# Performance work log

Measured on AMD Instinct MI355X. Metric: run time of the kernel, lower is better.

## Reference

```python
import jax, jax.numpy as jnp
import numpy as np

DIM = 256
NUM_HEADS = 4
HEAD_DIM = DIM // NUM_HEADS


def setup_inputs() -> dict:
    key = jax.random.key(0)
    ks = jax.random.split(key, 8)
    B, N, C = 4, 2048, DIM
    x = jax.random.normal(ks[0], (B, N, C), dtype=jnp.float32)
    R = jax.random.normal(ks[1], (B, 3, 3), dtype=jnp.float32)
    P = jax.random.normal(ks[2], (N, 3), dtype=jnp.float32)
    s = 1.0 / np.sqrt(C)
    qkv_w = jax.random.normal(ks[3], (3 * C, C), dtype=jnp.float32) * s
    qkv_b = jax.random.normal(ks[4], (3 * C,), dtype=jnp.float32) * 0.02
    proj_w = jax.random.normal(ks[5], (C, C), dtype=jnp.float32) * s
    proj_b = jax.random.normal(ks[6], (C,), dtype=jnp.float32) * 0.02
    pos_scale = jnp.asarray(1.0, dtype=jnp.float32)
    return {"x": x, "R": R, "P": P, "qkv_w": qkv_w, "qkv_b": qkv_b,
            "proj_w": proj_w, "proj_b": proj_b, "pos_scale": pos_scale}


def reference(x, R, P, qkv_w, qkv_b, proj_w, proj_b, pos_scale):
    B, N, C = x.shape
    H, D = NUM_HEADS, HEAD_DIM
    scale = D ** -0.5
    # qkv: (B,N,3C) -> (3,B,H,N,D)
    qkv = (x @ qkv_w.T + qkv_b).reshape(B, N, 3, H, D).transpose(2, 0, 3, 1, 4)
    q, k, v = qkv[0], qkv[1], qkv[2]
    # attention logits (B,H,N,N)
    attn = jnp.einsum('bhid,bhjd->bhij', q, k) * scale
    # positional bias: RP = (R @ P^T)^T -> (B,N,3); bias_ij = dot(RP_i, P_j)
    RP = jnp.einsum('bab,jb->bja', R, P) if False else jnp.einsum('bca,ja->bjc', jnp.swapaxes(R, 1, 2), P)
    RP = jnp.einsum('bcd,jd->bjc', R, P)  # (B,N,3): (R @ P.T).T
    bias = jnp.einsum('bik,jk->bij', RP, P)[:, None, :, :] * pos_scale  # (B,1,N,N) broadcast over heads
    attn = jax.nn.softmax(attn + bias, axis=-1)
    out = jnp.einsum('bhij,bhjd->bhid', attn, v)  # (B,H,N,D)
    out = out.transpose(0, 2, 1, 3).reshape(B, N, C)
    out = out @ proj_w.T + proj_b
    return out
```

## Files before the change

### kernel.cpp

```cpp
#include <hip/hip_runtime.h>
#include <hip/hip_bf16.h>

#define B_ 4
#define N_ 2048
#define C_ 256
#define H_ 4
#define D_ 64

typedef __attribute__((ext_vector_type(8))) short bf16x8;
typedef __attribute__((ext_vector_type(4))) float f32x4;

#define LOG2E 1.4426950408889634f

static __device__ inline unsigned short f2bf(float f) {
    unsigned u = __builtin_bit_cast(unsigned, f);
    unsigned r = (u + 0x7fffu + ((u >> 16) & 1u)) >> 16;
    return (unsigned short)r;
}
static __device__ inline float bf2f(unsigned short h) {
    unsigned u = ((unsigned)h) << 16;
    return __builtin_bit_cast(float, u);
}
static __device__ inline unsigned pack2(float a, float b) {
    __hip_bfloat162 h = __float22bfloat162_rn(make_float2(a, b));
    unsigned u;
    __builtin_memcpy(&u, &h, 4);
    return u;
}
static __device__ inline bf16x8 ld_frag(const unsigned short* p) {
    return __builtin_bit_cast(bf16x8, *(const uint4*)p);
}
static __device__ inline void gload_lds16(const unsigned short* g, unsigned short* l) {
    __builtin_amdgcn_global_load_lds(
        (const __attribute__((address_space(1))) unsigned int*)(g),
        (__attribute__((address_space(3))) unsigned int*)(l),
        16, 0, 0);
}
template<int CTRL>
static __device__ inline float fmax_dpp(float x) {
    int yi = __builtin_amdgcn_update_dpp(0, __builtin_bit_cast(int, x),
                                         CTRL, 0xf, 0xf, true);
    return fmaxf(x, __builtin_bit_cast(float, yi));
}

__global__ __launch_bounds__(256) void cvt_kernel(
    const float* __restrict__ x, const float* __restrict__ qkv_w,
    const float* __restrict__ proj_w, const float* __restrict__ Pm,
    unsigned short* __restrict__ xb, unsigned short* __restrict__ wqb,
    unsigned short* __restrict__ wpb, unsigned short* __restrict__ eb)
{
    const int bid = blockIdx.x, tid = threadIdx.x;
    if (bid >= 1152) {
        const int n = (bid - 1152) * 256 + tid;
        const float* pp = Pm + n * 3;
        float p0 = pp[0], p1 = pp[1], p2 = pp[2];
        unsigned u0 = f2bf(p0), u1 = f2bf(p1), u2 = f2bf(p2);
        unsigned v0 = f2bf(p0 - bf2f((unsigned short)u0));
        unsigned v1 = f2bf(p1 - bf2f((unsigned short)u1));
        unsigned v2 = f2bf(p2 - bf2f((unsigned short)u2));
        uint4 lo, hi;
        lo.x = u0 | (u1 << 16); lo.y = u2 | (v0 << 16);
        lo.z = v1 | (v2 << 16); lo.w = u0 | (u1 << 16);
        hi.x = u2; hi.y = 0u; hi.z = 0u; hi.w = 0u;
        *(uint4*)&eb[n * 16 + 0] = lo;
        *(uint4*)&eb[n * 16 + 8] = hi;
        return;
    }
    const float* s; unsigned short* d; int i;
    if (bid < 1024)      { s = x;      d = xb;  i = (bid * 256 + tid) * 8; }
    else if (bid < 1120) { s = qkv_w;  d = wqb; i = ((bid - 1024) * 256 + tid) * 8; }
    else                 { s = proj_w; d = wpb; i = ((bid - 1120) * 256 + tid) * 8; }
    float4 a = *(const float4*)(s + i);
    float4 b = *(const float4*)(s + i + 4);
    uint4 u;
    u.x = pack2(a.x, a.y); u.y = pack2(a.z, a.w);
    u.z = pack2(b.x, b.y); u.w = pack2(b.z, b.w);
    *(uint4*)(d + i) = u;
}

__global__ __launch_bounds__(256) void qkv_gemm(
    const unsigned short* __restrict__ xb, const unsigned short* __restrict__ wb,
    const float* __restrict__ bias, unsigned short* __restrict__ qb,
    unsigned short* __restrict__ kb, unsigned short* __restrict__ vt)
{
    __shared__ __align__(16) unsigned short As[2][128 * 64];
    __shared__ __align__(16) unsigned short Bs[2][128 * 64];
    const int m0 = blockIdx.x * 128, o0 = blockIdx.y * 128;
    const int tid = threadIdx.x;
    const int wave = tid >> 6, lane = tid & 63, quad = lane >> 4, l16 = lane & 15;
    const int wy = wave >> 1, wx = wave & 1;
    const int x7 = l16 & 7;
    const int rl = lane >> 3, sl = lane & 7;
    const int swz = (sl ^ rl) * 8;

    const unsigned short* aq0 = &xb[(size_t)(m0 + 32 * wave + rl) * 256 + swz];
    const unsigned short* bq0 = &wb[(size_t)(o0 + 32 * wave + rl) * 256 + swz];

    auto ISSUE = [&](int buf, int k0) {
        unsigned short* ad = &As[buf][(32 * wave) * 64];
        unsigned short* bd = &Bs[buf][(32 * wave) * 64];
        #pragma unroll
        for (int i = 0; i < 4; ++i) {
            gload_lds16(aq0 + (size_t)(8 * i) * 256 + k0, ad + (8 * i) * 64);
            gload_lds16(bq0 + (size_t)(8 * i) * 256 + k0, bd + (8 * i) * 64);
        }
    };

    f32x4 acc[4][4];
    #pragma unroll
    for (int i = 0; i < 4; ++i)
        #pragma unroll
        for (int j = 0; j < 4; ++j) acc[i][j] = (f32x4){0.f, 0.f, 0.f, 0.f};

    ISSUE(0, 0);

    #pragma unroll
    for (int t = 0; t < 4; ++t) {
        const int cur = t & 1;
        asm volatile("s_waitcnt vmcnt(0)" ::: "memory");
        __builtin_amdgcn_s_barrier();
        __builtin_amdgcn_sched_barrier(0);
        if (t < 3) ISSUE(cur ^ 1, (t + 1) * 64);
        __builtin_amdgcn_s_setprio(1);
        #pragma unroll
        for (int ks = 0; ks < 2; ++ks) {
            bf16x8 a[4], b[4];
            #pragma unroll
            for (int mt = 0; mt < 4; ++mt)
                a[mt] = ld_frag(&As[cur][(wy * 64 + mt * 16 + l16) * 64
                                         + (((ks * 4 + quad) ^ x7) * 8)]);
            #pragma unroll
            for (int nt = 0; nt < 4; ++nt)
                b[nt] = ld_frag(&Bs[cur][(wx * 64 + nt * 16 + l16) * 64
                                         + (((ks * 4 + quad) ^ x7) * 8)]);
            #pragma unroll
            for (int mt = 0; mt < 4; ++mt)
                #pragma unroll
                for (int nt = 0; nt < 4; ++nt)
                    acc[mt][nt] = __builtin_amdgcn_mfma_f32_16x16x32_bf16(a[mt], b[nt], acc[mt][nt], 0, 0, 0);
        }
        __builtin_amdgcn_s_setprio(0);
    }

    const int sec = o0 + wx * 64;
    const int three = sec >> 8;
    const int h = (sec >> 6) & 3;
    const int b = m0 >> 11;
    float bv[4];
    #pragma unroll
    for (int nt = 0; nt < 4; ++nt) bv[nt] = bias[sec + nt * 16 + l16];

    if (three == 2) {
        const int n64 = (m0 + wy * 64) & 2047;
        const size_t bh64 = ((size_t)b * H_ + h) * 64;
        #pragma unroll
        for (int nt = 0; nt < 4; ++nt) {
            int d = nt * 16 + l16;
            #pragma unroll
            for (int r = 0; r < 4; ++r) {
                ushort4 v;
                v.x = f2bf(acc[0][nt][r] + bv[nt]);
                v.y = f2bf(acc[1][nt][r] + bv[nt]);
                v.z = f2bf(acc[2][nt][r] + bv[nt]);
                v.w = f2bf(acc[3][nt][r] + bv[nt]);
                *(ushort4*)&vt[(bh64 + d) * N_ + n64 + 16 * quad + 4 * r] = v;
            }
        }
    } else {
        unsigned short* dst = (three == 0) ? qb : kb;
        float sc = (three == 0) ? (0.125f * LOG2E) : 1.0f;
        #pragma unroll
        for (int mt = 0; mt < 4; ++mt)
            #pragma unroll
            for (int r = 0; r < 4; ++r) {
                int n = (m0 + wy * 64 + mt * 16 + quad * 4 + r) & 2047;
                size_t rowbase = (((size_t)b * H_ + h) * N_ + n) * D_;
                #pragma unroll
                for (int nt = 0; nt < 4; ++nt)
                    dst[rowbase + nt * 16 + l16] = f2bf((acc[mt][nt][r] + bv[nt]) * sc);
            }
    }
}

#define LDK 64

__global__ __launch_bounds__(512) void attn_kernel(
    const unsigned short* __restrict__ qb, const unsigned short* __restrict__ kb,
    const unsigned short* __restrict__ vt, const unsigned short* __restrict__ eb,
    const float* __restrict__ Rm, const float* __restrict__ Pm,
    const float* __restrict__ ps_ptr,
    unsigned short* __restrict__ Opart, float* __restrict__ ml)
{
    __shared__ __align__(16) unsigned short Ks[2][64 * LDK];
    __shared__ __align__(16) unsigned short Vs[64 * LDK];
    __shared__ __align__(16) unsigned short Ps[128 * LDK];

    const int bh = blockIdx.y;
    const int b = bh >> 2;
    const int i0 = blockIdx.x * 128;
    const int split = blockIdx.z;
    const int tid = threadIdx.x;
    const int wave = tid >> 6, lane = tid & 63;
    const int quad = lane >> 4, l16 = lane & 15;
    const int x7 = l16 & 7;
    const float ps = ps_ptr[0];

    const size_t base = (size_t)bh * N_ * D_;
    const unsigned short* qg = qb + base;
    const unsigned short* kg = kb + base;
    const unsigned short* vg = vt + base;

    const int jbeg = split * (N_ / 4);

    const int rl = lane >> 3, sl = lane & 7;
    const int swz = (sl ^ rl) * 8;
    const unsigned short* kq = kg + (size_t)(jbeg + wave * 8 + rl) * D_ + swz;
    const unsigned short* vq = vg + (size_t)(wave * 8 + rl) * N_ + jbeg + swz;
    const unsigned short* ep = eb + (size_t)(jbeg + l16) * 16 + (quad & 1) * 8;

    auto ISSUE_K = [&](int nb) {
        gload_lds16(kq, &Ks[nb][(wave * 8) * LDK]);
        kq += 64 * D_;
    };
    auto ISSUE_V = [&]() {
        gload_lds16(vq, &Vs[(wave * 8) * LDK]);
        vq += 64;
    };
    bf16x8 e[4];
    auto LOAD_E = [&]() {
        #pragma unroll
        for (int t = 0; t < 4; ++t) e[t] = ld_frag(ep + t * 256);
        ep += 64 * 16;
    };

    ISSUE_K(0);
    LOAD_E();

    const int qrow = i0 + wave * 16 + l16;
    bf16x8 aq[3];
    #pragma unroll
    for (int ks = 0; ks < 2; ++ks)
        aq[ks] = ld_frag(&qg[(size_t)qrow * D_ + ks * 32 + quad * 8]);

    {
        float p0 = Pm[qrow * 3 + 0], p1 = Pm[qrow * 3 + 1], p2 = Pm[qrow * 3 + 2];
        float sc = ps * LOG2E;
        unsigned short ah[3], al[3];
        #pragma unroll
        for (int c = 0; c < 3; ++c) {
            float a = (Rm[b * 9 + c * 3 + 0] * p0 + Rm[b * 9 + c * 3 + 1] * p1
                     + Rm[b * 9 + c * 3 + 2] * p2) * sc;
            ah[c] = f2bf(a);
            al[c] = f2bf(a - bf2f(ah[c]));
        }
        bf16x8 ea = (bf16x8){0,0,0,0,0,0,0,0};
        if (quad == 0) {
            ea[0] = (short)ah[0]; ea[1] = (short)ah[1]; ea[2] = (short)ah[2];
            ea[3] = (short)ah[0]; ea[4] = (short)ah[1]; ea[5] = (short)ah[2];
            ea[6] = (short)al[0]; ea[7] = (short)al[1];
        } else if (quad == 1) {
            ea[0] = (short)al[2];
        }
        aq[2] = ea;
    }

    const bf16x8 ones = (bf16x8){0x3F80,0x3F80,0x3F80,0x3F80,0x3F80,0x3F80,0x3F80,0x3F80};

    float m_run = -1e30f;
    f32x4 o_acc[4], lacc;
    #pragma unroll
    for (int t = 0; t < 4; ++t) o_acc[t] = (f32x4){0.f, 0.f, 0.f, 0.f};
    lacc = (f32x4){0.f, 0.f, 0.f, 0.f};

    f32x4 sA[4], sB[4];

    auto S_COMPUTE = [&](f32x4 (&sc)[4], int kb_) {
        __builtin_amdgcn_s_setprio(1);
        #pragma unroll
        for (int t = 0; t < 4; ++t) {
            const int rb = (l16 + 16 * t) * LDK;
            f32x4 c = {0.f, 0.f, 0.f, 0.f};
            #pragma unroll
            for (int ks = 0; ks < 2; ++ks) {
                bf16x8 bk = ld_frag(&Ks[kb_][rb + (((ks * 4 + quad) ^ x7) * 8)]);
                c = __builtin_amdgcn_mfma_f32_16x16x32_bf16(aq[ks], bk, c, 0, 0, 0);
            }
            sc[t] = c;
        }
        #pragma unroll
        for (int t = 0; t < 4; ++t)
            sc[t] = __builtin_amdgcn_mfma_f32_16x16x32_bf16(aq[2], e[t], sc[t], 0, 0, 0);
        __builtin_amdgcn_s_setprio(0);
    };

    auto SOFTMAX = [&](f32x4 (&s)[4]) {
        float mt[4];
        #pragma unroll
        for (int t = 0; t < 4; ++t)
            mt[t] = fmaxf(fmaxf(fmaxf(s[t][0], s[t][1]), s[t][2]), s[t][3]);
        float mx = fmaxf(fmaxf(fmaxf(mt[0], mt[1]), mt[2]), mt[3]);
        mx = fmax_dpp<0xB1>(mx);
        mx = fmax_dpp<0x4E>(mx);
        mx = fmax_dpp<0x124>(mx);
        mx = fmax_dpp<0x128>(mx);
        if (__any(mx > m_run + 8.0f)) {
            float mnew = fmaxf(m_run, mx);
            float alpha = exp2f(m_run - mnew);
            #pragma unroll
            for (int t = 0; t < 4; ++t)
                #pragma unroll
                for (int r = 0; r < 4; ++r)
                    o_acc[t][r] *= alpha;
            #pragma unroll
            for (int r = 0; r < 4; ++r) lacc[r] *= alpha;
            m_run = mnew;
        }
        #pragma unroll
        for (int r = 0; r < 4; ++r) {
            float p0 = exp2f(s[0][r] - m_run), p1 = exp2f(s[1][r] - m_run);
            float p2 = exp2f(s[2][r] - m_run), p3 = exp2f(s[3][r] - m_run);
            uint2 w;
            w.x = pack2(p0, p1);
            w.y = pack2(p2, p3);
            const int prow = quad * 4 + r;
            *(uint2*)&Ps[(wave * 16 + prow) * LDK
                         + (((l16 >> 1) ^ (prow & 7)) * 8) + (l16 & 1) * 4] = w;
        }
    };

    auto PV = [&]() {
        __builtin_amdgcn_s_setprio(1);
        #pragma unroll
        for (int ks = 0; ks < 2; ++ks) {
            bf16x8 ap = ld_frag(&Ps[(wave * 16 + l16) * LDK
                                    + (((ks * 4 + quad) ^ x7) * 8)]);
            #pragma unroll
            for (int t = 0; t < 4; ++t) {
                bf16x8 bv = ld_frag(&Vs[(l16 + 16 * t) * LDK
                                        + (((ks * 4 + quad) ^ x7) * 8)]);
                o_acc[t] = __builtin_amdgcn_mfma_f32_16x16x32_bf16(ap, bv, o_acc[t], 0, 0, 0);
            }
            lacc = __builtin_amdgcn_mfma_f32_16x16x32_bf16(ap, ones, lacc, 0, 0, 0);
        }
        __builtin_amdgcn_s_setprio(0);
    };

    auto STEP = [&](int cur, bool more, f32x4 (&snew)[4], f32x4 (&sold)[4]) {
        asm volatile("s_waitcnt vmcnt(0)" ::: "memory");
        __builtin_amdgcn_s_barrier();
        __builtin_amdgcn_sched_barrier(0);
        LOAD_E();
        ISSUE_V();
        if (more) ISSUE_K(cur ^ 1);
        __builtin_amdgcn_sched_barrier(0);
        SOFTMAX(sold);
        S_COMPUTE(snew, cur);
        __builtin_amdgcn_sched_barrier(0);
        if (more) asm volatile("s_waitcnt vmcnt(1)" ::: "memory");
        else      asm volatile("s_waitcnt vmcnt(0)" ::: "memory");
        __builtin_amdgcn_s_barrier();
        __builtin_amdgcn_sched_barrier(0);
        PV();
    };

    asm volatile("s_waitcnt vmcnt(0)" ::: "memory");
    __builtin_amdgcn_s_barrier();
    __builtin_amdgcn_sched_barrier(0);
    ISSUE_K(1);
    S_COMPUTE(sA, 0);

    #pragma unroll 1
    for (int it = 0; it < 3; ++it) {
        STEP(1, true, sB, sA);
        STEP(0, true, sA, sB);
    }
    STEP(1, false, sB, sA);

    asm volatile("s_waitcnt vmcnt(0)" ::: "memory");
    __builtin_amdgcn_s_barrier();
    __builtin_amdgcn_sched_barrier(0);
    ISSUE_V();
    SOFTMAX(sB);
    asm volatile("s_waitcnt vmcnt(0)" ::: "memory");
    __builtin_amdgcn_s_barrier();
    __builtin_amdgcn_sched_barrier(0);
    PV();

    const size_t pbase = (size_t)(split * 16 + bh) * N_;
    #pragma unroll
    for (int r = 0; r < 4; ++r) {
        int row = i0 + wave * 16 + quad * 4 + r;
        #pragma unroll
        for (int t = 0; t < 4; ++t)
            Opart[(pbase + row) * D_ + l16 + 16 * t] = f2bf(o_acc[t][r]);
        if (l16 == 0) {
            float2* mlp = (float2*)ml;
            mlp[pbase + row] = make_float2(m_run, lacc[r]);
        }
    }
}

__global__ __launch_bounds__(256) void proj_gemm(
    const unsigned short* __restrict__ Opart, const float* __restrict__ ml,
    const unsigned short* __restrict__ wb, const float* __restrict__ bias,
    float* __restrict__ out)
{
    __shared__ __align__(16) unsigned short As[2][64 * 64];
    __shared__ __align__(16) unsigned short Bs[2][64 * 64];
    const int m0 = blockIdx.x * 64, o0 = blockIdx.y * 64;
    const int tid = threadIdx.x;
    const int wave = tid >> 6, lane = tid & 63, quad = lane >> 4, l16 = lane & 15;
    const int x7 = l16 & 7;
    const int rl = lane >> 3, sl = lane & 7;
    const int swz = (sl ^ rl) * 8;
    const float2* mlp = (const float2*)ml;

    const int srow = tid >> 2, sc16 = (tid & 3) * 16;
    const int s0 = (tid & 3) * 2;
    const int sm = m0 + srow, sb = sm >> 11, sn = sm & 2047;

    float wgt[4][4];
    #pragma unroll
    for (int h = 0; h < 4; ++h) {
        size_t r1 = (size_t)(sb * 4 + h) * N_ + sn;
        float2 m0v = mlp[r1], m1v = mlp[r1 + 16 * N_];
        float2 m2v = mlp[r1 + 32 * N_], m3v = mlp[r1 + 48 * N_];
        float mm = fmaxf(fmaxf(m0v.x, m1v.x), fmaxf(m2v.x, m3v.x));
        float w0 = exp2f(m0v.x - mm), w1 = exp2f(m1v.x - mm);
        float w2 = exp2f(m2v.x - mm), w3 = exp2f(m3v.x - mm);
        float inv = 1.f / (m0v.y * w0 + m1v.y * w1 + m2v.y * w2 + m3v.y * w3);
        wgt[h][0] = w0 * inv; wgt[h][1] = w1 * inv;
        wgt[h][2] = w2 * inv; wgt[h][3] = w3 * inv;
    }

    const unsigned short* bq0 = &wb[(size_t)(o0 + 16 * wave + rl) * 256 + swz];
    auto ISSUE_B = [&](int buf, int k0) {
        unsigned short* bd = &Bs[buf][(16 * wave) * 64];
        gload_lds16(bq0 + k0,           bd);
        gload_lds16(bq0 + 8 * 256 + k0, bd + 8 * 64);
    };

    union U16 { uint4 u; unsigned short s[8]; };
    U16 ar[4][2];
    auto LOAD_A = [&](int h) {
        size_t r1 = (size_t)(sb * 4 + h) * N_ + sn;
        #pragma unroll
        for (int s = 0; s < 4; ++s) {
            const unsigned short* p = &Opart[(r1 + (size_t)(16 * s) * N_) * D_ + sc16];
            ar[s][0].u = *(const uint4*)(p);
            ar[s][1].u = *(const uint4*)(p + 8);
        }
    };

    ISSUE_B(0, 0);
    LOAD_A(0);

    f32x4 acc[4];
    #pragma unroll
    for (int j = 0; j < 4; ++j) acc[j] = (f32x4){0.f, 0.f, 0.f, 0.f};

    #pragma unroll
    for (int t = 0; t < 4; ++t) {
        const int cur = t & 1;
        {
            float w0 = wgt[t][0], w1 = wgt[t][1], w2 = wgt[t][2], w3 = wgt[t][3];
            #pragma unroll
            for (int j = 0; j < 2; ++j) {
                uint4 mv;
                unsigned* mp = (unsigned*)&mv;
                #pragma unroll
                for (int q = 0; q < 4; ++q) {
                    float lo = bf2f(ar[0][j].s[2*q])   * w0 + bf2f(ar[1][j].s[2*q])   * w1
                             + bf2f(ar[2][j].s[2*q])   * w2 + bf2f(ar[3][j].s[2*q])   * w3;
                    float hi = bf2f(ar[0][j].s[2*q+1]) * w0 + bf2f(ar[1][j].s[2*q+1]) * w1
                             + bf2f(ar[2][j].s[2*q+1]) * w2 + bf2f(ar[3][j].s[2*q+1]) * w3;
                    mp[q] = pack2(lo, hi);
                }
                *(uint4*)&As[cur][srow * 64 + (((s0 + j) ^ (srow & 7)) * 8)] = mv;
            }
        }
        __syncthreads();
        if (t < 3) {
            ISSUE_B(cur ^ 1, (t + 1) * 64);
            LOAD_A(t + 1);
        }
        __builtin_amdgcn_s_setprio(1);
        #pragma unroll
        for (int ks = 0; ks < 2; ++ks) {
            bf16x8 a = ld_frag(&As[cur][(wave * 16 + l16) * 64
                                        + (((ks * 4 + quad) ^ x7) * 8)]);
            #pragma unroll
            for (int nt = 0; nt < 4; ++nt) {
                bf16x8 b = ld_frag(&Bs[cur][(nt * 16 + l16) * 64
                                            + (((ks * 4 + quad) ^ x7) * 8)]);
                acc[nt] = __builtin_amdgcn_mfma_f32_16x16x32_bf16(a, b, acc[nt], 0, 0, 0);
            }
        }
        __builtin_amdgcn_s_setprio(0);
    }

    float bv[4];
    #pragma unroll
    for (int nt = 0; nt < 4; ++nt) bv[nt] = bias[o0 + nt * 16 + l16];
    #pragma unroll
    for (int r = 0; r < 4; ++r) {
        int m = m0 + wave * 16 + quad * 4 + r;
        #pragma unroll
        for (int nt = 0; nt < 4; ++nt)
            out[(size_t)m * 256 + o0 + nt * 16 + l16] = acc[nt][r] + bv[nt];
    }
}

extern "C" void kernel_launch(void* const* d_in, const int* in_sizes, int n_in,
                              void* d_out, int out_size, void* d_ws, size_t ws_size,
                              hipStream_t stream) {
    const float* x       = (const float*)d_in[0];
    const float* Rm      = (const float*)d_in[1];
    const float* Pm      = (const float*)d_in[2];
    const float* qkv_w   = (const float*)d_in[3];
    const float* qkv_b   = (const float*)d_in[4];
    const float* proj_w  = (const float*)d_in[5];
    const float* proj_b  = (const float*)d_in[6];
    const float* pos_scl = (const float*)d_in[7];
    float* out = (float*)d_out;

    const size_t NE = (size_t)B_ * H_ * N_ * D_;
    unsigned short* opart = (unsigned short*)d_ws;
    unsigned short* qb    = opart + 4 * NE;
    unsigned short* kb    = qb   + NE;
    unsigned short* vtb   = kb   + NE;
    float*          mlb   = (float*)(vtb + NE);
    unsigned short* eb    = (unsigned short*)(mlb + (size_t)4 * 16 * N_ * 2);
    unsigned short* wqb   = eb  + 2048 * 16;
    unsigned short* wpb   = wqb + 768 * 256;
    unsigned short* xb    = opart;

    cvt_kernel<<<1160, 256, 0, stream>>>(x, qkv_w, proj_w, Pm, xb, wqb, wpb, eb);
    qkv_gemm<<<dim3(64, 6), 256, 0, stream>>>(xb, wqb, qkv_b, qb, kb, vtb);
    attn_kernel<<<dim3(16, 16, 4), 512, 0, stream>>>(qb, kb, vtb, eb, Rm, Pm, pos_scl, opart, mlb);
    proj_gemm<<<dim3(128, 4), 256, 0, stream>>>(opart, mlb, wpb, proj_b, out);
}
```

Before: 131.8 us.

## Double KV tile to 128 keys and halve attention split-K count

The attention kernel now processes 128 keys per iteration instead of 64, with larger K/V/P shared buffers and twice the score fragments per wave. The split-K factor drops from 4 to 2, so the grid is half as large and the proj_gemm merge combines only two partial outputs. This cuts loop and barrier overhead and partial-output traffic, but adds register and LDS pressure and leaves fewer blocks to fill the device.

```diff
diff --git a/kernel.cpp b/kernel.cpp
--- a/kernel.cpp
+++ b/kernel.cpp
@@ -183,6 +183,7 @@
 }
 
 #define LDK 64
+#define LDP 128
 
 __global__ __launch_bounds__(512) void attn_kernel(
     const unsigned short* __restrict__ qb, const unsigned short* __restrict__ kb,
@@ -191,9 +192,9 @@
     const float* __restrict__ ps_ptr,
     unsigned short* __restrict__ Opart, float* __restrict__ ml)
 {
-    __shared__ __align__(16) unsigned short Ks[2][64 * LDK];
-    __shared__ __align__(16) unsigned short Vs[64 * LDK];
-    __shared__ __align__(16) unsigned short Ps[128 * LDK];
+    __shared__ __align__(16) unsigned short Ks[2][128 * LDK];
+    __shared__ __align__(16) unsigned short Vs[64 * LDP];
+    __shared__ __align__(16) unsigned short Ps[128 * LDP];
 
     const int bh = blockIdx.y;
     const int b = bh >> 2;
@@ -210,31 +211,33 @@
     const unsigned short* kg = kb + base;
     const unsigned short* vg = vt + base;
 
-    const int jbeg = split * (N_ / 4);
+    const int jbeg = split * (N_ / 2);
 
     const int rl = lane >> 3, sl = lane & 7;
-    const int swz = (sl ^ rl) * 8;
-    const unsigned short* kq = kg + (size_t)(jbeg + wave * 8 + rl) * D_ + swz;
-    const unsigned short* vq = vg + (size_t)(wave * 8 + rl) * N_ + jbeg + swz;
+    const unsigned short* kp = kg + (size_t)(jbeg + wave * 16 + rl) * D_ + (sl ^ rl) * 8;
+    const int rv = lane >> 4, sv = lane & 15;
+    const unsigned short* vp0 = vg + (size_t)(wave * 8 + rv) * N_ + jbeg + (sv ^ rv) * 8;
+    const unsigned short* vp1 = vg + (size_t)(wave * 8 + 4 + rv) * N_ + jbeg + (sv ^ (4 + rv)) * 8;
     const unsigned short* ep = eb + (size_t)(jbeg + l16) * 16 + (quad & 1) * 8;
 
     auto ISSUE_K = [&](int nb) {
-        gload_lds16(kq, &Ks[nb][(wave * 8) * LDK]);
-        kq += 64 * D_;
+        gload_lds16(kp,          &Ks[nb][(wave * 16) * LDK]);
+        gload_lds16(kp + 8 * D_, &Ks[nb][(wave * 16 + 8) * LDK]);
+        kp += 128 * D_;
     };
     auto ISSUE_V = [&]() {
-        gload_lds16(vq, &Vs[(wave * 8) * LDK]);
-        vq += 64;
-    };
-    bf16x8 e[4];
+        gload_lds16(vp0, &Vs[(wave * 8) * LDP]);
+        gload_lds16(vp1, &Vs[(wave * 8 + 4) * LDP]);
+        vp0 += 128; vp1 += 128;
+    };
+    bf16x8 e[8];
     auto LOAD_E = [&]() {
         #pragma unroll
-        for (int t = 0; t < 4; ++t) e[t] = ld_frag(ep + t * 256);
-        ep += 64 * 16;
+        for (int t = 0; t < 8; ++t) e[t] = ld_frag(ep + t * 256);
+        ep += 128 * 16;
     };
 
     ISSUE_K(0);
-    LOAD_E();
 
     const int qrow = i0 + wave * 16 + l16;
     bf16x8 aq[3];
@@ -272,12 +275,12 @@
     for (int t = 0; t < 4; ++t) o_acc[t] = (f32x4){0.f, 0.f, 0.f, 0.f};
     lacc = (f32x4){0.f, 0.f, 0.f, 0.f};
 
-    f32x4 sA[4], sB[4];
-
-    auto S_COMPUTE = [&](f32x4 (&sc)[4], int kb_) {
+    f32x4 sA[8], sB[8];
+
+    auto S_COMPUTE = [&](f32x4 (&sc)[8], int kb_) {
         __builtin_amdgcn_s_setprio(1);
         #pragma unroll
-        for (int t = 0; t < 4; ++t) {
+        for (int t = 0; t < 8; ++t) {
             const int rb = (l16 + 16 * t) * LDK;
             f32x4 c = {0.f, 0.f, 0.f, 0.f};
             #pragma unroll
@@ -288,17 +291,19 @@
             sc[t] = c;
         }
         #pragma unroll
-        for (int t = 0; t < 4; ++t)
+        for (int t = 0; t < 8; ++t)
             sc[t] = __builtin_amdgcn_mfma_f32_16x16x32_bf16(aq[2], e[t], sc[t], 0, 0, 0);
         __builtin_amdgcn_s_setprio(0);
     };
 
-    auto SOFTMAX = [&](f32x4 (&s)[4]) {
-        float mt[4];
-        #pragma unroll
-        for (int t = 0; t < 4; ++t)
+    auto SOFTMAX = [&](f32x4 (&s)[8]) {
+        float mt[8];
+        #pragma unroll
+        for (int t = 0; t < 8; ++t)
             mt[t] = fmaxf(fmaxf(fmaxf(s[t][0], s[t][1]), s[t][2]), s[t][3]);
-        float mx = fmaxf(fmaxf(fmaxf(mt[0], mt[1]), mt[2]), mt[3]);
+        float mx = mt[0];
+        #pragma unroll
+        for (int t = 1; t < 8; ++t) mx = fmaxf(mx, mt[t]);
         mx = fmax_dpp<0xB1>(mx);
         mx = fmax_dpp<0x4E>(mx);
         mx = fmax_dpp<0x124>(mx);
@@ -319,24 +324,28 @@
         for (int r = 0; r < 4; ++r) {
             float p0 = exp2f(s[0][r] - m_run), p1 = exp2f(s[1][r] - m_run);
             float p2 = exp2f(s[2][r] - m_run), p3 = exp2f(s[3][r] - m_run);
-            uint2 w;
-            w.x = pack2(p0, p1);
-            w.y = pack2(p2, p3);
+            float p4 = exp2f(s[4][r] - m_run), p5 = exp2f(s[5][r] - m_run);
+            float p6 = exp2f(s[6][r] - m_run), p7 = exp2f(s[7][r] - m_run);
+            uint2 w0, w1;
+            w0.x = pack2(p0, p1); w0.y = pack2(p2, p3);
+            w1.x = pack2(p4, p5); w1.y = pack2(p6, p7);
             const int prow = quad * 4 + r;
-            *(uint2*)&Ps[(wave * 16 + prow) * LDK
-                         + (((l16 >> 1) ^ (prow & 7)) * 8) + (l16 & 1) * 4] = w;
+            const int a0 = (wave * 16 + prow) * LDP
+                         + (((l16 >> 1) ^ (prow & 7)) * 8) + (l16 & 1) * 4;
+            *(uint2*)&Ps[a0] = w0;
+            *(uint2*)&Ps[a0 + 64] = w1;
         }
     };
 
     auto PV = [&]() {
         __builtin_amdgcn_s_setprio(1);
         #pragma unroll
-        for (int ks = 0; ks < 2; ++ks) {
-            bf16x8 ap = ld_frag(&Ps[(wave * 16 + l16) * LDK
+        for (int ks = 0; ks < 4; ++ks) {
+            bf16x8 ap = ld_frag(&Ps[(wave * 16 + l16) * LDP
                                     + (((ks * 4 + quad) ^ x7) * 8)]);
             #pragma unroll
             for (int t = 0; t < 4; ++t) {
-                bf16x8 bv = ld_frag(&Vs[(l16 + 16 * t) * LDK
+                bf16x8 bv = ld_frag(&Vs[(l16 + 16 * t) * LDP
                                         + (((ks * 4 + quad) ^ x7) * 8)]);
                 o_acc[t] = __builtin_amdgcn_mfma_f32_16x16x32_bf16(ap, bv, o_acc[t], 0, 0, 0);
             }
@@ -345,18 +354,19 @@
         __builtin_amdgcn_s_setprio(0);
     };
 
-    auto STEP = [&](int cur, bool more, f32x4 (&snew)[4], f32x4 (&sold)[4]) {
+    auto STEP = [&](int cur, bool more, f32x4 (&snew)[8], f32x4 (&sold)[8]) {
         asm volatile("s_waitcnt vmcnt(0)" ::: "memory");
         __builtin_amdgcn_s_barrier();
         __builtin_amdgcn_sched_barrier(0);
         LOAD_E();
         ISSUE_V();
+        __builtin_amdgcn_sched_barrier(0);
         if (more) ISSUE_K(cur ^ 1);
         __builtin_amdgcn_sched_barrier(0);
         SOFTMAX(sold);
         S_COMPUTE(snew, cur);
         __builtin_amdgcn_sched_barrier(0);
-        if (more) asm volatile("s_waitcnt vmcnt(1)" ::: "memory");
+        if (more) asm volatile("s_waitcnt vmcnt(2)" ::: "memory");
         else      asm volatile("s_waitcnt vmcnt(0)" ::: "memory");
         __builtin_amdgcn_s_barrier();
         __builtin_amdgcn_sched_barrier(0);
@@ -366,7 +376,9 @@
     asm volatile("s_waitcnt vmcnt(0)" ::: "memory");
     __builtin_amdgcn_s_barrier();
     __builtin_amdgcn_sched_barrier(0);
+    LOAD_E();
     ISSUE_K(1);
+    __builtin_amdgcn_sched_barrier(0);
     S_COMPUTE(sA, 0);
 
     #pragma unroll 1
@@ -419,18 +431,15 @@
     const int s0 = (tid & 3) * 2;
     const int sm = m0 + srow, sb = sm >> 11, sn = sm & 2047;
 
-    float wgt[4][4];
+    float wgt[4][2];
     #pragma unroll
     for (int h = 0; h < 4; ++h) {
         size_t r1 = (size_t)(sb * 4 + h) * N_ + sn;
         float2 m0v = mlp[r1], m1v = mlp[r1 + 16 * N_];
-        float2 m2v = mlp[r1 + 32 * N_], m3v = mlp[r1 + 48 * N_];
-        float mm = fmaxf(fmaxf(m0v.x, m1v.x), fmaxf(m2v.x, m3v.x));
+        float mm = fmaxf(m0v.x, m1v.x);
         float w0 = exp2f(m0v.x - mm), w1 = exp2f(m1v.x - mm);
-        float w2 = exp2f(m2v.x - mm), w3 = exp2f(m3v.x - mm);
-        float inv = 1.f / (m0v.y * w0 + m1v.y * w1 + m2v.y * w2 + m3v.y * w3);
+        float inv = 1.f / (m0v.y * w0 + m1v.y * w1);
         wgt[h][0] = w0 * inv; wgt[h][1] = w1 * inv;
-        wgt[h][2] = w2 * inv; wgt[h][3] = w3 * inv;
     }
 
     const unsigned short* bq0 = &wb[(size_t)(o0 + 16 * wave + rl) * 256 + swz];
@@ -441,11 +450,11 @@
     };
 
     union U16 { uint4 u; unsigned short s[8]; };
-    U16 ar[4][2];
+    U16 ar[2][2];
     auto LOAD_A = [&](int h) {
         size_t r1 = (size_t)(sb * 4 + h) * N_ + sn;
         #pragma unroll
-        for (int s = 0; s < 4; ++s) {
+        for (int s = 0; s < 2; ++s) {
             const unsigned short* p = &Opart[(r1 + (size_t)(16 * s) * N_) * D_ + sc16];
             ar[s][0].u = *(const uint4*)(p);
             ar[s][1].u = *(const uint4*)(p + 8);
@@ -463,17 +472,15 @@
     for (int t = 0; t < 4; ++t) {
         const int cur = t & 1;
         {
-            float w0 = wgt[t][0], w1 = wgt[t][1], w2 = wgt[t][2], w3 = wgt[t][3];
+            float w0 = wgt[t][0], w1 = wgt[t][1];
             #pragma unroll
             for (int j = 0; j < 2; ++j) {
                 uint4 mv;
                 unsigned* mp = (unsigned*)&mv;
                 #pragma unroll
                 for (int q = 0; q < 4; ++q) {
-                    float lo = bf2f(ar[0][j].s[2*q])   * w0 + bf2f(ar[1][j].s[2*q])   * w1
-                             + bf2f(ar[2][j].s[2*q])   * w2 + bf2f(ar[3][j].s[2*q])   * w3;
-                    float hi = bf2f(ar[0][j].s[2*q+1]) * w0 + bf2f(ar[1][j].s[2*q+1]) * w1
-                             + bf2f(ar[2][j].s[2*q+1]) * w2 + bf2f(ar[3][j].s[2*q+1]) * w3;
+                    float lo = bf2f(ar[0][j].s[2*q])   * w0 + bf2f(ar[1][j].s[2*q])   * w1;
+                    float hi = bf2f(ar[0][j].s[2*q+1]) * w0 + bf2f(ar[1][j].s[2*q+1]) * w1;
                     mp[q] = pack2(lo, hi);
                 }
                 *(uint4*)&As[cur][srow * 64 + (((s0 + j) ^ (srow & 7)) * 8)] = mv;
@@ -526,17 +533,17 @@
 
     const size_t NE = (size_t)B_ * H_ * N_ * D_;
     unsigned short* opart = (unsigned short*)d_ws;
-    unsigned short* qb    = opart + 4 * NE;
+    unsigned short* qb    = opart + 2 * NE;
     unsigned short* kb    = qb   + NE;
     unsigned short* vtb   = kb   + NE;
     float*          mlb   = (float*)(vtb + NE);
-    unsigned short* eb    = (unsigned short*)(mlb + (size_t)4 * 16 * N_ * 2);
+    unsigned short* eb    = (unsigned short*)(mlb + (size_t)2 * 16 * N_ * 2);
     unsigned short* wqb   = eb  + 2048 * 16;
     unsigned short* wpb   = wqb + 768 * 256;
     unsigned short* xb    = opart;
 
     cvt_kernel<<<1160, 256, 0, stream>>>(x, qkv_w, proj_w, Pm, xb, wqb, wpb, eb);
     qkv_gemm<<<dim3(64, 6), 256, 0, stream>>>(xb, wqb, qkv_b, qb, kb, vtb);
-    attn_kernel<<<dim3(16, 16, 4), 512, 0, stream>>>(qb, kb, vtb, eb, Rm, Pm, pos_scl, opart, mlb);
+    attn_kernel<<<dim3(16, 16, 2), 512, 0, stream>>>(qb, kb, vtb, eb, Rm, Pm, pos_scl, opart, mlb);
     proj_gemm<<<dim3(128, 4), 256, 0, stream>>>(opart, mlb, wpb, proj_b, out);
 }
```

Measured after the change: 140.1 us. 6.3% more time.
